# Kernel tuning notes

Hardware: AMD Instinct MI355X
Metric: run time of the kernel (lower is better)

Reference implementation:

```python
import jax, jax.numpy as jnp
import numpy as np

PATCH = 4
WINDOW = 4
MAX_ROUNDS = 4
MIN_ROUNDS = 2
LAMBDA_P = 0.2
TOPK = 8


def _ln(x, g, b, eps=1e-5):
    m = x.mean(-1, keepdims=True)
    v = ((x - m) ** 2).mean(-1, keepdims=True)
    return (x - m) / jnp.sqrt(v + eps) * g + b


def _mlp(x, w1, b1, w2, b2):
    # Linear -> exact GELU -> Linear (matches nn.GELU default)
    return jax.nn.gelu(x @ w1 + b1, approximate=False) @ w2 + b2


def setup_inputs() -> dict:
    key = jax.random.key(0)
    ks = jax.random.split(key, 24)
    B, T, D, V = 16, 4096, 256, 256
    s = 0.02
    w = lambda i, shape: jax.random.normal(ks[i], shape, jnp.float32) * s
    z = lambda *shape: jnp.zeros(shape, jnp.float32)
    o = lambda *shape: jnp.ones(shape, jnp.float32)
    return {
        'x': jax.random.randint(ks[0], (B, T), 0, V),
        'emb': w(1, (V, D)), 'pos': w(2, (PATCH, D)),
        'gru_wih': w(3, (D, 3 * D)), 'gru_whh': w(4, (D, 3 * D)),
        'gru_bih': z(3 * D), 'gru_bhh': z(3 * D),
        'ln_p_g': o(D), 'ln_p_b': z(D),
        'sum_w': w(5, (D, D)), 'sum_b': z(D),
        'msg_w1': w(6, (2 * D, D)), 'msg_b1': z(D), 'msg_w2': w(7, (D, D)), 'msg_b2': z(D),
        'upd_w1': w(8, (2 * D, D)), 'upd_b1': z(D), 'upd_w2': w(9, (D, D)), 'upd_b2': z(D),
        'halt_w': w(10, (D, 1)), 'halt_b': z(1),
        'ln_mp_g': o(D), 'ln_mp_b': z(D),
        'q_w': w(11, (D, D)), 'q_b': z(D),
        'k_w': w(12, (D, D)), 'k_b': z(D),
        'v_w': w(13, (D, D)), 'v_b': z(D),
        'o_w': w(14, (D, D)), 'o_b': z(D),
        'bc_w': w(15, (D, D)), 'bc_b': z(D),
        'ln_f_g': o(D), 'ln_f_b': z(D),
        'head_w': w(16, (D, V)),
    }


def reference(x, emb, pos, gru_wih, gru_whh, gru_bih, gru_bhh, ln_p_g, ln_p_b,
              sum_w, sum_b, msg_w1, msg_b1, msg_w2, msg_b2, upd_w1, upd_b1,
              upd_w2, upd_b2, halt_w, halt_b, ln_mp_g, ln_mp_b, q_w, q_b,
              k_w, k_b, v_w, v_b, o_w, o_b, bc_w, bc_b, ln_f_g, ln_f_b, head_w):
    B, T = x.shape
    D = emb.shape[1]
    Np = T // PATCH  # T is divisible by PATCH for these shapes (no pad needed)

    # --- GRU patch processor over B*Np sequences of length PATCH ---
    tok = x.reshape(B * Np, PATCH)
    hseq = emb[tok] + pos[None]  # [BN, P, D]

    def gru_step(h, xt):
        gi = xt @ gru_wih + gru_bih
        gh = h @ gru_whh + gru_bhh
        ir, iz, inn = jnp.split(gi, 3, -1)
        hr, hz, hn = jnp.split(gh, 3, -1)
        r = jax.nn.sigmoid(ir + hr)
        zz = jax.nn.sigmoid(iz + hz)
        n = jnp.tanh(inn + r * hn)
        h = (1 - zz) * n + zz * h
        return h, h

    h0 = jnp.zeros((B * Np, D), hseq.dtype)
    _, gout = jax.lax.scan(gru_step, h0, jnp.swapaxes(hseq, 0, 1))
    local = _ln(jnp.swapaxes(gout, 0, 1), ln_p_g, ln_p_b).reshape(B, Np, PATCH, D)
    summaries = local.mean(2) @ sum_w + sum_b  # [B, Np, D]

    # --- Local message passing with ACT-style halting (fixed MAX_ROUNDS) ---
    h = summaries
    remaining = jnp.ones((B, Np, 1), h.dtype)
    out_mp = jnp.zeros_like(h)
    kl = jnp.zeros((), h.dtype)
    for step in range(MAX_ROUNDS):
        padded = jnp.pad(h, ((0, 0), (WINDOW, 0), (0, 0)))
        # neighbors: self plus previous WINDOW patches -> [B, Np, W+1, D]
        neigh = jnp.stack([padded[:, WINDOW - w:WINDOW - w + Np] for w in range(WINDOW + 1)], axis=2)
        self_exp = jnp.broadcast_to(h[:, :, None, :], neigh.shape)
        msgs = _mlp(jnp.concatenate([self_exp, neigh], -1), msg_w1, msg_b1, msg_w2, msg_b2).mean(2)
        h = _ln(h + _mlp(jnp.concatenate([h, msgs], -1), upd_w1, upd_b1, upd_w2, upd_b2), ln_mp_g, ln_mp_b)
        if step < MIN_ROUNDS:
            hp = jnp.zeros((B, Np, 1), h.dtype)
        else:
            hp = jax.nn.sigmoid(h.mean(1, keepdims=True) @ halt_w + halt_b)  # [B,1,1]
            hp = jnp.broadcast_to(hp, (B, Np, 1))
        if step == MAX_ROUNDS - 1:
            hp = jnp.ones_like(hp)
        out_mp = out_mp + remaining * hp * h
        remaining = remaining * (1 - hp)
        p_geom = LAMBDA_P * (1 - LAMBDA_P) ** step
        # F.kl_div(log(mean+eps), log(p_geom), log_target=True) = p*(log p - log(mean+eps))
        kl = kl + p_geom * (np.log(p_geom) - jnp.log(hp.mean() + 1e-8))
    kl = kl / MAX_ROUNDS

    # --- Sparse top-k causal retrieval ---
    q = out_mp @ q_w + q_b
    kk = out_mp @ k_w + k_b
    v = out_mp @ v_w + v_b
    scores = jnp.einsum('bnd,bmd->bnm', q, kk) / np.sqrt(D).astype(np.float32)
    causal = jnp.tril(jnp.ones((Np, Np), bool))
    neg = jnp.asarray(-jnp.inf, scores.dtype)
    scores = jnp.where(causal[None], scores, neg)
    vals, idx = jax.lax.top_k(scores, TOPK)  # [B, Np, k]
    bi = jnp.arange(B)[:, None, None]
    ni = jnp.arange(Np)[None, :, None]
    sparse = jnp.full_like(scores, neg).at[bi, ni, idx].set(vals)
    attn = jax.nn.softmax(sparse, axis=-1)
    retrieved = jnp.einsum('bnm,bmd->bnd', attn, v) @ o_w + o_b

    # --- Broadcast back to tokens and project ---
    combined = out_mp + retrieved
    broad = combined @ bc_w + bc_b
    final = (local + broad[:, :, None, :]).reshape(B, Np * PATCH, D)[:, :T]
    logits = _ln(final, ln_f_g, ln_f_b) @ head_w
    return logits, kl
```

## Files before the change

### kernel.cpp

```cpp
#include <hip/hip_runtime.h>
#include <math.h>


typedef __bf16 bf16_t;
typedef bf16_t bf16x8 __attribute__((ext_vector_type(8)));
typedef bf16_t bf16x4 __attribute__((ext_vector_type(4)));
typedef float f32x4 __attribute__((ext_vector_type(4)));

#define GF_BIAS 1
#define GF_GELU 4
#define GF_RES 8
#define GF_F32OUT 32

__device__ __forceinline__ float gelu_exact(float x) {
  return 0.5f * x * (1.0f + erff(x * 0.7071067811865475f));
}

__device__ __forceinline__ float sigm(float x) { return 1.f / (1.f + expf(-x)); }

__device__ __forceinline__ float wave_sum(float v) {
#pragma unroll
  for (int o = 32; o; o >>= 1) v += __shfl_xor(v, o, 64);
  return v;
}

__device__ __forceinline__ void gload16(const void* g, void* l) {
  __builtin_amdgcn_global_load_lds(
      (const __attribute__((address_space(1))) void*)g,
      (__attribute__((address_space(3))) void*)l, 16, 0, 0);
}

__device__ __forceinline__ unsigned long long skey(float s, int m) {
  unsigned u = __float_as_uint(s);
  u ^= (u & 0x80000000u) ? 0xFFFFFFFFu : 0x80000000u;
  return ((unsigned long long)u << 32) | (unsigned)(0x7FFFFFFF - m);
}

template<int FLAGS>
__global__ __launch_bounds__(256)
void gemm_bt(const bf16_t* __restrict__ A, const bf16_t* __restrict__ Bt,
             void* __restrict__ Cv, const float* __restrict__ bias,
             const bf16_t* __restrict__ res,
             int lda, int ldb, int ldc, int ldr)
{
  __shared__ __align__(16) bf16_t As[128][64];
  __shared__ __align__(16) bf16_t Bs[128][64];
  const int m0 = blockIdx.x * 128, n0 = blockIdx.y * 128;
  const int tid = threadIdx.x, lane = tid & 63, wave = tid >> 6;
  const int wm = (wave >> 1) << 6, wn = (wave & 1) << 6;
  const int lr = lane & 15, lg = lane >> 4;
  const int cx = lane & 7;

  const int srow = wave * 32 + (lane >> 3);
  const int scol = (((lane & 7) ^ ((lane >> 3) & 7)) * 8);
  const bf16_t* ga = A  + (long long)(m0 + srow) * lda + scol;
  const bf16_t* gb = Bt + (long long)(n0 + srow) * ldb + scol;
  char* lA = (char*)(&As[srow][0]) + (lane & 7) * 16;
  char* lB = (char*)(&Bs[srow][0]) + (lane & 7) * 16;

  f32x4 acc[4][4] = {};

#pragma unroll
  for (int kt = 0; kt < 4; kt++) {
    const int ko = kt * 64;
#pragma unroll
    for (int q = 0; q < 4; q++) {
      gload16(ga + (long long)q * 8 * lda + ko, lA + q * 1024);
      gload16(gb + (long long)q * 8 * ldb + ko, lB + q * 1024);
    }
    __syncthreads();
#pragma unroll
    for (int kk = 0; kk < 2; kk++) {
      const int co = ((kk * 4 + lg) ^ cx) << 4;
      bf16x8 af[4], bfv[4];
#pragma unroll
      for (int i = 0; i < 4; i++)
        af[i]  = *(const bf16x8*)((char*)As + (wm + i * 16 + lr) * 128 + co);
#pragma unroll
      for (int j = 0; j < 4; j++)
        bfv[j] = *(const bf16x8*)((char*)Bs + (wn + j * 16 + lr) * 128 + co);
#pragma unroll
      for (int i = 0; i < 4; i++)
#pragma unroll
        for (int j = 0; j < 4; j++)
          acc[i][j] = __builtin_amdgcn_mfma_f32_16x16x32_bf16(af[i], bfv[j], acc[i][j], 0, 0, 0);
    }
    if (kt < 3) __syncthreads();
  }

#pragma unroll
  for (int i = 0; i < 4; i++) {
#pragma unroll
    for (int j = 0; j < 4; j++) {
      const int col = n0 + wn + j * 16 + lr;
      const float bval = (FLAGS & GF_BIAS) ? bias[col] : 0.f;
#pragma unroll
      for (int e = 0; e < 4; e++) {
        const int row = m0 + wm + i * 16 + lg * 4 + e;
        float v = acc[i][j][e] + bval;
        if (FLAGS & GF_RES) v += (float)res[(long long)row * ldr + col];
        if (FLAGS & GF_GELU) v = gelu_exact(v);
        const long long ci = (long long)row * ldc + col;
        if (FLAGS & GF_F32OUT) ((float*)Cv)[ci] = v;
        else                   ((bf16_t*)Cv)[ci] = (bf16_t)v;
      }
    }
  }
}

template<int FLAGS>
__global__ __launch_bounds__(256)
void gemm64(const bf16_t* __restrict__ A, const bf16_t* __restrict__ Bt,
            void* __restrict__ Cv, const float* __restrict__ bias,
            const bf16_t* __restrict__ res,
            int lda, int ldb, int ldc, int ldr)
{
  __shared__ __align__(16) bf16_t As[64][64];
  __shared__ __align__(16) bf16_t Bs[64][64];
  const int m0 = blockIdx.x * 64, n0 = blockIdx.y * 64;
  const int tid = threadIdx.x, lane = tid & 63, wave = tid >> 6;
  const int wm = (wave >> 1) * 32, wn = (wave & 1) * 32;
  const int lr = lane & 15, lg = lane >> 4;
  const int cx = lane & 7;

  const int srow = tid >> 3;
  const int scol = (((tid & 7) ^ (srow & 7)) * 8);
  const bf16_t* ga = A  + (long long)(m0 + srow) * lda + scol;
  const bf16_t* gb = Bt + (long long)(n0 + srow) * ldb + scol;
  char* lA = (char*)As + tid * 16;
  char* lB = (char*)Bs + tid * 16;

  f32x4 acc[2][2] = {};

#pragma unroll
  for (int kt = 0; kt < 4; kt++) {
    const int ko = kt * 64;
    gload16(ga + ko, lA);
    gload16(ga + 32LL * lda + ko, lA + 4096);
    gload16(gb + ko, lB);
    gload16(gb + 32LL * ldb + ko, lB + 4096);
    __syncthreads();
#pragma unroll
    for (int kk = 0; kk < 2; kk++) {
      const int co = ((kk * 4 + lg) ^ cx) << 4;
      bf16x8 af[2], bfv[2];
#pragma unroll
      for (int i = 0; i < 2; i++)
        af[i]  = *(const bf16x8*)((char*)As + (wm + i * 16 + lr) * 128 + co);
#pragma unroll
      for (int j = 0; j < 2; j++)
        bfv[j] = *(const bf16x8*)((char*)Bs + (wn + j * 16 + lr) * 128 + co);
#pragma unroll
      for (int i = 0; i < 2; i++)
#pragma unroll
        for (int j = 0; j < 2; j++)
          acc[i][j] = __builtin_amdgcn_mfma_f32_16x16x32_bf16(af[i], bfv[j], acc[i][j], 0, 0, 0);
    }
    if (kt < 3) __syncthreads();
  }

#pragma unroll
  for (int i = 0; i < 2; i++) {
#pragma unroll
    for (int j = 0; j < 2; j++) {
      const int col = n0 + wn + j * 16 + lr;
      const float bval = (FLAGS & GF_BIAS) ? bias[col] : 0.f;
#pragma unroll
      for (int e = 0; e < 4; e++) {
        const int row = m0 + wm + i * 16 + lg * 4 + e;
        float v = acc[i][j][e] + bval;
        if (FLAGS & GF_RES) v += (float)res[(long long)row * ldr + col];
        if (FLAGS & GF_GELU) v = gelu_exact(v);
        const long long ci = (long long)row * ldc + col;
        if (FLAGS & GF_F32OUT) ((float*)Cv)[ci] = v;
        else                   ((bf16_t*)Cv)[ci] = (bf16_t)v;
      }
    }
  }
}

__global__ __launch_bounds__(64)
void k_fatopk(const bf16_t* __restrict__ QKV, bf16_t* __restrict__ O) {
  const int b = blockIdx.y;
  const int qw = (int)((blockIdx.x + ((blockIdx.y * 21) & 63)) & 63);
  const int lane = threadIdx.x;
  const int lr = lane & 15, lg = lane >> 4;
  const bf16_t* Qp = QKV + (long long)b * (1024LL * 768);
  const bf16_t* Kp = Qp + 256;
  const bf16_t* Vp = Qp + 512;
  const int q0 = qw * 16;
  const int qrow = q0 + lr;

  bf16x8 bq[8];
#pragma unroll
  for (int s = 0; s < 8; s++)
    bq[s] = *(const bf16x8*)(Qp + (long long)qrow * 768 + s * 32 + lg * 8);

  unsigned long long kv[8] = {0ull, 0ull, 0ull, 0ull, 0ull, 0ull, 0ull, 0ull};

#define INS8(KEY) {                                                     \
    const unsigned long long k_ = (KEY);                                \
    if (k_ > kv[7]) {                                                   \
      kv[7] = k_;                                                       \
      _Pragma("unroll")                                                 \
      for (int j_ = 7; j_ > 0; j_--)                                    \
        if (kv[j_] > kv[j_-1]) {                                        \
          const unsigned long long t_ = kv[j_];                         \
          kv[j_] = kv[j_-1]; kv[j_-1] = t_;                             \
        }                                                               \
    }                                                                   \
  }

  const int klim = qw + 1;
  for (int kt = 0; kt < klim; kt += 2) {
    const int kt2 = (kt + 1 < klim) ? kt + 1 : kt;
    const bf16_t* ka = Kp + (long long)(kt  * 16 + lr) * 768 + lg * 8;
    const bf16_t* kb = Kp + (long long)(kt2 * 16 + lr) * 768 + lg * 8;
    bf16x8 afA[8], afB[8];
#pragma unroll
    for (int s = 0; s < 8; s++) afA[s] = *(const bf16x8*)(ka + s * 32);
#pragma unroll
    for (int s = 0; s < 8; s++) afB[s] = *(const bf16x8*)(kb + s * 32);
    f32x4 a0 = {}, a1 = {};
#pragma unroll
    for (int s = 0; s < 8; s += 2) {
      a0 = __builtin_amdgcn_mfma_f32_16x16x32_bf16(afA[s],     bq[s],     a0, 0, 0, 0);
      a1 = __builtin_amdgcn_mfma_f32_16x16x32_bf16(afA[s + 1], bq[s + 1], a1, 0, 0, 0);
    }
#pragma unroll
    for (int e = 0; e < 4; e++) {
      const int m = kt * 16 + lg * 4 + e;
      if (m <= qrow) INS8(skey((a0[e] + a1[e]) * 0.0625f, m));
    }
    if (kt2 != kt) {
      f32x4 b0 = {}, b1 = {};
#pragma unroll
      for (int s = 0; s < 8; s += 2) {
        b0 = __builtin_amdgcn_mfma_f32_16x16x32_bf16(afB[s],     bq[s],     b0, 0, 0, 0);
        b1 = __builtin_amdgcn_mfma_f32_16x16x32_bf16(afB[s + 1], bq[s + 1], b1, 0, 0, 0);
      }
#pragma unroll
      for (int e = 0; e < 4; e++) {
        const int m = kt2 * 16 + lg * 4 + e;
        if (m <= qrow) INS8(skey((b0[e] + b1[e]) * 0.0625f, m));
      }
    }
  }
#undef INS8

  float wv[8]; int wi[8];
#pragma unroll
  for (int r = 0; r < 8; r++) {
    unsigned long long mk = kv[0];
    unsigned long long ok = __shfl_xor(mk, 16, 64); if (ok > mk) mk = ok;
    ok = __shfl_xor(mk, 32, 64); if (ok > mk) mk = ok;
    if (mk != 0ull) {
      unsigned hi = (unsigned)(mk >> 32);
      hi ^= (hi & 0x80000000u) ? 0x80000000u : 0xFFFFFFFFu;
      wv[r] = __uint_as_float(hi);
      wi[r] = 0x7FFFFFFF - (int)(unsigned)(mk & 0xFFFFFFFFu);
    } else {
      wv[r] = 0.f; wi[r] = -1;
    }
    if (kv[0] == mk && mk != 0ull) {
#pragma unroll
      for (int j = 0; j < 7; j++) kv[j] = kv[j + 1];
      kv[7] = 0ull;
    }
  }

  const float mx = wv[0];
  float w8[8]; float den = 0.f;
#pragma unroll
  for (int j = 0; j < 8; j++) {
    w8[j] = (wi[j] >= 0) ? expf(wv[j] - mx) : 0.f;
    den += w8[j];
  }
  const float inv = 1.f / den;

  f32x4 av[16] = {};
#pragma unroll
  for (int j = 0; j < 8; j++) {
    if (wi[j] >= 0) {
      const float wj = w8[j] * inv;
      const bf16_t* vr = Vp + (long long)wi[j] * 768 + lg * 64;
#pragma unroll
      for (int c = 0; c < 8; c++) {
        const bf16x8 vv = *(const bf16x8*)(vr + c * 8);
#pragma unroll
        for (int e = 0; e < 4; e++) {
          av[2 * c][e]     = fmaf(wj, (float)vv[e],     av[2 * c][e]);
          av[2 * c + 1][e] = fmaf(wj, (float)vv[4 + e], av[2 * c + 1][e]);
        }
      }
    }
  }
  bf16_t* op = O + ((long long)b * 1024 + qrow) * 256 + lg * 64;
#pragma unroll
  for (int c = 0; c < 8; c++) {
    bf16x8 ov;
#pragma unroll
    for (int e = 0; e < 4; e++) {
      ov[e]     = (bf16_t)av[2 * c][e];
      ov[4 + e] = (bf16_t)av[2 * c + 1][e];
    }
    *(bf16x8*)(op + c * 8) = ov;
  }
}

struct TD { const float* src; bf16_t* dst; int N; int k0; int ld; };
struct PrepArgs {
  TD d[16];
  const float* emb; const float* pos; bf16_t* XE;
  const float* msg_b1; const float* msg_b2; const float* upd_w1; const float* upd_b1;
  const float* q_b; const float* k_b; const float* v_b;
  float* BIAS3; float* QKVB;
};

__global__ __launch_bounds__(256) void k_prep(PrepArgs pa) {
  const int y = blockIdx.y, x = blockIdx.x, d = threadIdx.x;
  if (y < 16) {
    TD t = pa.d[y];
    if (x >= t.N) return;
    if (t.k0 < 0) t.dst[(long long)x * 256 + d] = (bf16_t)t.src[(long long)x * t.ld + d];
    else          t.dst[(long long)x * 256 + d] = (bf16_t)t.src[(long long)(t.k0 + d) * t.ld + x];
  } else if (y == 16) {
    const int p = x >> 8, v = x & 255;
    pa.XE[(long long)x * 256 + d] = (bf16_t)(pa.emb[v * 256 + d] + pa.pos[p * 256 + d]);
  } else {
    if      (x == 0) pa.BIAS3[d] = pa.msg_b1[d];
    else if (x == 1) pa.BIAS3[256 + d] = 0.f;
    else if (x == 2) {
      float acc = pa.upd_b1[d];
      for (int k = 0; k < 256; k++) acc += pa.msg_b2[k] * pa.upd_w1[(long long)(256 + k) * 256 + d];
      pa.BIAS3[512 + d] = acc;
    }
    else if (x == 3) pa.QKVB[d] = pa.q_b[d];
    else if (x == 4) pa.QKVB[256 + d] = pa.k_b[d];
    else if (x == 5) pa.QKVB[512 + d] = pa.v_b[d];
  }
}

__global__ __launch_bounds__(64)
void k_gru_gate(const int* __restrict__ x, const bf16_t* __restrict__ gitab,
                const bf16_t* __restrict__ GH, const float* __restrict__ bhh,
                bf16_t* __restrict__ H, bf16_t* __restrict__ LOC, int t)
{
  const int s = blockIdx.x, lane = threadIdx.x, d0 = lane * 4;
  const int v = x[s * 4 + t];
  const bf16_t* gi = gitab + (long long)(t * 256 + v) * 768;
  const bf16x4 g_r = *(const bf16x4*)(gi + d0);
  const bf16x4 g_z = *(const bf16x4*)(gi + 256 + d0);
  const bf16x4 g_n = *(const bf16x4*)(gi + 512 + d0);
  float hr[4], hz[4], hn[4], hp[4];
  if (t == 0) {
#pragma unroll
    for (int e = 0; e < 4; e++) {
      hr[e] = bhh[d0 + e]; hz[e] = bhh[256 + d0 + e]; hn[e] = bhh[512 + d0 + e];
      hp[e] = 0.f;
    }
  } else {
    const bf16_t* gh = GH + (long long)s * 768;
    const bf16x4 a = *(const bf16x4*)(gh + d0);
    const bf16x4 b4 = *(const bf16x4*)(gh + 256 + d0);
    const bf16x4 c4 = *(const bf16x4*)(gh + 512 + d0);
    const bf16x4 hv = *(const bf16x4*)(H + (long long)s * 256 + d0);
#pragma unroll
    for (int e = 0; e < 4; e++) { hr[e] = a[e]; hz[e] = b4[e]; hn[e] = c4[e]; hp[e] = hv[e]; }
  }
  bf16x4 ho;
#pragma unroll
  for (int e = 0; e < 4; e++) {
    const float r = sigm((float)g_r[e] + hr[e]);
    const float zz = sigm((float)g_z[e] + hz[e]);
    const float nn = tanhf((float)g_n[e] + r * hn[e]);
    ho[e] = (bf16_t)((1.f - zz) * nn + zz * hp[e]);
  }
  *(bf16x4*)(H + (long long)s * 256 + d0) = ho;
  *(bf16x4*)(LOC + ((long long)s * 4 + t) * 256 + d0) = ho;
}

__global__ __launch_bounds__(64)
void k_ln(const bf16_t* __restrict__ X, const bf16_t* __restrict__ ADD, int addmode,
          bf16_t* __restrict__ OUT, const float* __restrict__ g,
          const float* __restrict__ b)
{
  const long long r = blockIdx.x;
  const int d0 = threadIdx.x * 4;
  const bf16x4 xv = *(const bf16x4*)(X + r * 256 + d0);
  float xf[4];
#pragma unroll
  for (int e = 0; e < 4; e++) xf[e] = (float)xv[e];
  if (addmode == 1) {
    const bf16x4 av = *(const bf16x4*)(ADD + r * 256 + d0);
#pragma unroll
    for (int e = 0; e < 4; e++) xf[e] += (float)av[e];
  } else if (addmode == 2) {
    const bf16x4 av = *(const bf16x4*)(ADD + (r >> 2) * 256 + d0);
#pragma unroll
    for (int e = 0; e < 4; e++) xf[e] += (float)av[e];
  }
  const float mean = wave_sum(xf[0] + xf[1] + xf[2] + xf[3]) * (1.f / 256.f);
  float q = 0.f;
#pragma unroll
  for (int e = 0; e < 4; e++) { const float dx = xf[e] - mean; q += dx * dx; }
  const float rstd = rsqrtf(wave_sum(q) * (1.f / 256.f) + 1e-5f);
  const float4 gv = *(const float4*)(g + d0);
  const float4 bv = *(const float4*)(b + d0);
  const float gg[4] = {gv.x, gv.y, gv.z, gv.w};
  const float bb[4] = {bv.x, bv.y, bv.z, bv.w};
  bf16x4 ov;
#pragma unroll
  for (int e = 0; e < 4; e++) ov[e] = (bf16_t)((xf[e] - mean) * rstd * gg[e] + bb[e]);
  *(bf16x4*)(OUT + r * 256 + d0) = ov;
}

__global__ __launch_bounds__(64)
void k_lnp4(bf16_t* __restrict__ LOC, bf16_t* __restrict__ SUMB,
            const float* __restrict__ g, const float* __restrict__ b)
{
  const long long s = blockIdx.x;
  const int d0 = threadIdx.x * 4;
  const float4 gv = *(const float4*)(g + d0);
  const float4 bv = *(const float4*)(b + d0);
  const float gg[4] = {gv.x, gv.y, gv.z, gv.w};
  const float bb[4] = {bv.x, bv.y, bv.z, bv.w};
  float accd[4] = {0.f, 0.f, 0.f, 0.f};
#pragma unroll
  for (int t = 0; t < 4; t++) {
    bf16_t* row = LOC + (s * 4 + t) * 256 + d0;
    const bf16x4 xv = *(const bf16x4*)row;
    float xf[4];
#pragma unroll
    for (int e = 0; e < 4; e++) xf[e] = (float)xv[e];
    const float mean = wave_sum(xf[0] + xf[1] + xf[2] + xf[3]) * (1.f / 256.f);
    float q = 0.f;
#pragma unroll
    for (int e = 0; e < 4; e++) { const float dx = xf[e] - mean; q += dx * dx; }
    const float rstd = rsqrtf(wave_sum(q) * (1.f / 256.f) + 1e-5f);
    bf16x4 ov;
#pragma unroll
    for (int e = 0; e < 4; e++) {
      const float y = (xf[e] - mean) * rstd * gg[e] + bb[e];
      ov[e] = (bf16_t)y;
      accd[e] += y;
    }
    *(bf16x4*)row = ov;
  }
  bf16x4 sv;
#pragma unroll
  for (int e = 0; e < 4; e++) sv[e] = (bf16_t)(accd[e] * 0.25f);
  *(bf16x4*)(SUMB + s * 256 + d0) = sv;
}

__global__ __launch_bounds__(64)
void k_gelumix(const bf16_t* __restrict__ A3, bf16_t* __restrict__ G)
{
  const long long s = blockIdx.x;
  const int n = (int)(s & 1023);
  const int d0 = threadIdx.x * 4;
  const bf16x4 av = *(const bf16x4*)(A3 + s * 768 + d0);
  float a[4];
#pragma unroll
  for (int e = 0; e < 4; e++) a[e] = (float)av[e];
  float acc[4] = {0.f, 0.f, 0.f, 0.f};
  const bf16_t* bbase = A3 + s * 768 + 256 + d0;
#pragma unroll
  for (int w = 0; w <= 4; w++) {
    if (n >= w) {
      const bf16x4 bn = *(const bf16x4*)(bbase - (long long)w * 768);
#pragma unroll
      for (int e = 0; e < 4; e++) acc[e] += gelu_exact(a[e] + (float)bn[e]);
    } else {
#pragma unroll
      for (int e = 0; e < 4; e++) acc[e] += gelu_exact(a[e]);
    }
  }
  bf16x4 ov;
#pragma unroll
  for (int e = 0; e < 4; e++) ov[e] = (bf16_t)(acc[e] * 0.2f);
  *(bf16x4*)(G + s * 256 + d0) = ov;
}

__global__ __launch_bounds__(64)
void k_halt1(const bf16_t* __restrict__ Hm, float* __restrict__ PS) {
  const int c = blockIdx.x, b = blockIdx.y, d0 = threadIdx.x * 4;
  float acc[4] = {0.f, 0.f, 0.f, 0.f};
  const bf16_t* base = Hm + ((long long)b * 1024 + c * 32) * 256 + d0;
#pragma unroll 4
  for (int n = 0; n < 32; n++) {
    const bf16x4 hv = *(const bf16x4*)(base + (long long)n * 256);
#pragma unroll
    for (int e = 0; e < 4; e++) acc[e] += (float)hv[e];
  }
  float4 o4; o4.x = acc[0]; o4.y = acc[1]; o4.z = acc[2]; o4.w = acc[3];
  *(float4*)(PS + ((long long)b * 32 + c) * 256 + d0) = o4;
}

__global__ __launch_bounds__(64)
void k_halt2(const float* __restrict__ PS, const float* __restrict__ hw,
             const float* __restrict__ hb, float* __restrict__ HP) {
  const int b = blockIdx.x, d0 = threadIdx.x * 4;
  float acc[4] = {0.f, 0.f, 0.f, 0.f};
  for (int c = 0; c < 32; c++) {
    const float4 p4 = *(const float4*)(PS + ((long long)b * 32 + c) * 256 + d0);
    acc[0] += p4.x; acc[1] += p4.y; acc[2] += p4.z; acc[3] += p4.w;
  }
  const float4 w4 = *(const float4*)(hw + d0);
  float val = (acc[0] * w4.x + acc[1] * w4.y + acc[2] * w4.z + acc[3] * w4.w) * (1.f / 1024.f);
  val = wave_sum(val);
  if (threadIdx.x == 0) HP[b] = sigm(val + hb[0]);
}

__global__ void k_kl(const float* __restrict__ HP, float* __restrict__ out) {
  float s = 0.f;
  for (int b = 0; b < 16; b++) s += HP[b];
  const float hpm = s * (1.f / 16.f);
  const float l8 = logf(1e-8f);
  const float p0 = 0.2f, p1 = 0.16f, p2 = 0.128f, p3 = 0.1024f;
  const float kl = p0 * (logf(p0) - l8)
                 + p1 * (logf(p1) - l8)
                 + p2 * (logf(p2) - logf(hpm + 1e-8f))
                 + p3 * (logf(p3) - logf(1.f + 1e-8f));
  out[0] = kl * 0.25f;
}

__global__ __launch_bounds__(64)
void k_outmp(const bf16_t* __restrict__ Hm, const float* __restrict__ HP,
             bf16_t* __restrict__ O, int acc) {
  const long long s = blockIdx.x;
  const int d0 = threadIdx.x * 4;
  const int b = (int)(s >> 10);
  const float hp = HP[b];
  const bf16x4 hv = *(const bf16x4*)(Hm + s * 256 + d0);
  bf16x4 ov;
  if (acc) {
    const bf16x4 pv = *(const bf16x4*)(O + s * 256 + d0);
#pragma unroll
    for (int e = 0; e < 4; e++) ov[e] = (bf16_t)((float)pv[e] + (1.f - hp) * (float)hv[e]);
  } else {
#pragma unroll
    for (int e = 0; e < 4; e++) ov[e] = (bf16_t)(hp * (float)hv[e]);
  }
  *(bf16x4*)(O + s * 256 + d0) = ov;
}

extern "C" void kernel_launch(void* const* d_in, const int* in_sizes, int n_in,
                              void* d_out, int out_size, void* d_ws, size_t ws_size,
                              hipStream_t stream) {
  (void)in_sizes; (void)n_in; (void)ws_size;
  const int*   x      = (const int*)d_in[0];
  const float* emb    = (const float*)d_in[1];
  const float* pos    = (const float*)d_in[2];
  const float* wih    = (const float*)d_in[3];
  const float* whh    = (const float*)d_in[4];
  const float* bih    = (const float*)d_in[5];
  const float* bhh    = (const float*)d_in[6];
  const float* lnp_g  = (const float*)d_in[7];
  const float* lnp_b  = (const float*)d_in[8];
  const float* sum_w  = (const float*)d_in[9];
  const float* sum_b  = (const float*)d_in[10];
  const float* msg_w1 = (const float*)d_in[11];
  const float* msg_b1 = (const float*)d_in[12];
  const float* msg_w2 = (const float*)d_in[13];
  const float* msg_b2 = (const float*)d_in[14];
  const float* upd_w1 = (const float*)d_in[15];
  const float* upd_b1 = (const float*)d_in[16];
  const float* upd_w2 = (const float*)d_in[17];
  const float* upd_b2 = (const float*)d_in[18];
  const float* halt_w = (const float*)d_in[19];
  const float* halt_b = (const float*)d_in[20];
  const float* lnm_g  = (const float*)d_in[21];
  const float* lnm_b  = (const float*)d_in[22];
  const float* q_b    = (const float*)d_in[24];
  const float* k_b    = (const float*)d_in[26];
  const float* v_b    = (const float*)d_in[28];
  const float* o_b    = (const float*)d_in[30];
  const float* bc_b   = (const float*)d_in[32];
  const float* lnf_g  = (const float*)d_in[33];
  const float* lnf_b  = (const float*)d_in[34];

  char* base = (char*)d_ws;
  size_t off = 0;
  auto alloc = [&](size_t bytes) -> void* {
    void* p = (void*)(base + off);
    off += (bytes + 255) & ~(size_t)255;
    return p;
  };
  const size_t SL2 = 16384ull * 256 * 2;
  bf16_t* WIHT  = (bf16_t*)alloc(768 * 256 * 2);
  bf16_t* WHHT  = (bf16_t*)alloc(768 * 256 * 2);
  bf16_t* SUMT  = (bf16_t*)alloc(256 * 256 * 2);
  bf16_t* MW    = (bf16_t*)alloc(768 * 256 * 2);
  bf16_t* W2T   = (bf16_t*)alloc(256 * 256 * 2);
  bf16_t* W2NT  = (bf16_t*)alloc(256 * 256 * 2);
  bf16_t* UW1MT = (bf16_t*)alloc(256 * 256 * 2);
  bf16_t* UW2T  = (bf16_t*)alloc(256 * 256 * 2);
  bf16_t* WCB   = (bf16_t*)alloc(256 * 256 * 2);
  bf16_t* QKVW  = (bf16_t*)alloc(768 * 256 * 2);
  bf16_t* OT    = (bf16_t*)alloc(256 * 256 * 2);
  bf16_t* BCT   = (bf16_t*)alloc(256 * 256 * 2);
  bf16_t* HEADT = (bf16_t*)alloc(256 * 256 * 2);
  float*  BIAS3 = (float*)alloc(768 * 4);
  float*  QKVB  = (float*)alloc(768 * 4);
  bf16_t* XE    = (bf16_t*)alloc(1024ull * 256 * 2);
  bf16_t* GITAB = (bf16_t*)alloc(1024ull * 768 * 2);
  bf16_t* LOCb  = (bf16_t*)alloc(65536ull * 256 * 2);

  char*   SCR   = (char*)alloc(16ull * 1024 * 1024 * 4);
  bf16_t* GH    = (bf16_t*)SCR;
  bf16_t* H     = (bf16_t*)(SCR + 25165824);
  bf16_t* SUMB  = (bf16_t*)(SCR + 33554432);
  bf16_t* A3    = (bf16_t*)(SCR + 41943040);

  bf16_t* HMP   = (bf16_t*)alloc(SL2);
  bf16_t* G     = (bf16_t*)alloc(SL2);
  bf16_t* BROAD = (bf16_t*)alloc(SL2);
  bf16_t* UB    = (bf16_t*)alloc(SL2);
  bf16_t* U2B   = (bf16_t*)alloc(SL2);
  bf16_t* OUTMP = (bf16_t*)alloc(SL2);
  bf16_t* QKV   = (bf16_t*)alloc(16384ull * 768 * 2);
  float*  PS    = (float*)alloc(512ull * 256 * 4);
  float*  HP    = (float*)alloc(64);
  bf16_t* ATT   = UB;
  bf16_t* COMB  = U2B;
  float*  out   = (float*)d_out;
  float*  klout = out + (out_size - 1);

  PrepArgs pa;
  pa.d[0]  = { wih,                    WIHT,            768, 0,   768 };
  pa.d[1]  = { whh,                    WHHT,            768, 0,   768 };
  pa.d[2]  = { sum_w,                  SUMT,            256, 0,   256 };
  pa.d[3]  = { msg_w1,                 MW,              256, 0,   256 };
  pa.d[4]  = { msg_w1,                 MW + 256 * 256,  256, 256, 256 };
  pa.d[5]  = { upd_w1,                 MW + 512 * 256,  256, 0,   256 };
  pa.d[6]  = { msg_w2,                 W2T,             256, 0,   256 };
  pa.d[7]  = { upd_w1,                 UW1MT,           256, 256, 256 };
  pa.d[8]  = { upd_w2,                 UW2T,            256, 0,   256 };
  pa.d[9]  = { (const float*)d_in[23], QKVW,            256, 0,   256 };
  pa.d[10] = { (const float*)d_in[25], QKVW + 256*256,  256, 0,   256 };
  pa.d[11] = { (const float*)d_in[27], QKVW + 512*256,  256, 0,   256 };
  pa.d[12] = { (const float*)d_in[29], OT,              256, 0,   256 };
  pa.d[13] = { (const float*)d_in[31], BCT,             256, 0,   256 };
  pa.d[14] = { (const float*)d_in[35], HEADT,           256, 0,   256 };
  pa.d[15] = { msg_w2,                 W2NT,            256, -1,  256 };
  pa.emb = emb; pa.pos = pos; pa.XE = XE;
  pa.msg_b1 = msg_b1; pa.msg_b2 = msg_b2; pa.upd_w1 = upd_w1; pa.upd_b1 = upd_b1;
  pa.q_b = q_b; pa.k_b = k_b; pa.v_b = v_b;
  pa.BIAS3 = BIAS3; pa.QKVB = QKVB;
  k_prep<<<dim3(1024, 18), 256, 0, stream>>>(pa);

  gemm64<0><<<dim3(4, 4), 256, 0, stream>>>(
      UW1MT, W2NT, WCB, nullptr, nullptr, 256, 256, 256, 0);

  gemm64<GF_BIAS><<<dim3(16, 12), 256, 0, stream>>>(
      XE, WIHT, GITAB, bih, nullptr, 256, 256, 768, 0);

  k_gru_gate<<<16384, 64, 0, stream>>>(x, GITAB, GH, bhh, H, LOCb, 0);
  for (int t = 1; t < 4; t++) {
    gemm_bt<GF_BIAS><<<dim3(128, 6), 256, 0, stream>>>(
        H, WHHT, GH, bhh, nullptr, 256, 256, 768, 0);
    k_gru_gate<<<16384, 64, 0, stream>>>(x, GITAB, GH, bhh, H, LOCb, t);
  }

  k_lnp4<<<16384, 64, 0, stream>>>(LOCb, SUMB, lnp_g, lnp_b);
  gemm64<GF_BIAS><<<dim3(256, 4), 256, 0, stream>>>(
      SUMB, SUMT, HMP, sum_b, nullptr, 256, 256, 256, 0);

  for (int step = 0; step < 4; step++) {
    gemm_bt<GF_BIAS><<<dim3(128, 6), 256, 0, stream>>>(
        HMP, MW, A3, BIAS3, nullptr, 256, 256, 768, 0);
    k_gelumix<<<16384, 64, 0, stream>>>(A3, G);
    gemm64<GF_RES | GF_GELU><<<dim3(256, 4), 256, 0, stream>>>(
        G, WCB, UB, nullptr, A3 + 512, 256, 256, 256, 768);
    gemm64<GF_BIAS><<<dim3(256, 4), 256, 0, stream>>>(
        UB, UW2T, U2B, upd_b2, nullptr, 256, 256, 256, 0);
    k_ln<<<16384, 64, 0, stream>>>(HMP, U2B, 1, HMP, lnm_g, lnm_b);
    if (step == 2) {
      k_halt1<<<dim3(32, 16), 64, 0, stream>>>(HMP, PS);
      k_halt2<<<16, 64, 0, stream>>>(PS, halt_w, halt_b, HP);
      k_kl<<<1, 1, 0, stream>>>(HP, klout);
      k_outmp<<<16384, 64, 0, stream>>>(HMP, HP, OUTMP, 0);
    } else if (step == 3) {
      k_outmp<<<16384, 64, 0, stream>>>(HMP, HP, OUTMP, 1);
    }
  }

  gemm_bt<GF_BIAS><<<dim3(128, 6), 256, 0, stream>>>(
      OUTMP, QKVW, QKV, QKVB, nullptr, 256, 256, 768, 0);
  k_fatopk<<<dim3(64, 16), 64, 0, stream>>>(QKV, ATT);
  gemm64<GF_BIAS | GF_RES><<<dim3(256, 4), 256, 0, stream>>>(
      ATT, OT, COMB, o_b, OUTMP, 256, 256, 256, 256);
  gemm64<GF_BIAS><<<dim3(256, 4), 256, 0, stream>>>(
      COMB, BCT, BROAD, bc_b, nullptr, 256, 256, 256, 0);

  k_ln<<<65536, 64, 0, stream>>>(LOCb, BROAD, 2, LOCb, lnf_g, lnf_b);
  gemm_bt<GF_F32OUT><<<dim3(512, 2), 256, 0, stream>>>(
      LOCb, HEADT, out, nullptr, nullptr, 256, 256, 256, 0);
}
```

Measured before the change: 487.5 us.

## Split top-k attention key scan across four waves and fuse final layer-norm with output mix

The top-k retrieval kernel now runs four waves per 16-query block. Each wave scans an interleaved subset of key tiles and keeps its own top-8 candidates, and the per-wave lists are merged through shared memory by one wave. The value gather is then spread across all 256 threads. This shortens the serial causal key loop, which is badly load-imbalanced for late query blocks. Separately, the last message-passing step fuses its layer norm with the out_mp accumulation, so the HMP write and reread plus one launch are dropped. The cost is extra syncthreads and shared-memory merge work.

```diff
diff --git a/kernel.cpp b/kernel.cpp
--- a/kernel.cpp
+++ b/kernel.cpp
@@ -179,11 +179,16 @@
   }
 }
 
-__global__ __launch_bounds__(64)
+__global__ __launch_bounds__(256)
 void k_fatopk(const bf16_t* __restrict__ QKV, bf16_t* __restrict__ O) {
+  __shared__ unsigned long long cand[4][16][8];
+  __shared__ float wrow[16][8];
+  __shared__ int   irow[16][8];
   const int b = blockIdx.y;
-  const int qw = (int)((blockIdx.x + ((blockIdx.y * 21) & 63)) & 63);
-  const int lane = threadIdx.x;
+  const int qw = (int)((blockIdx.x + ((unsigned)(b * 21) & 63u)) & 63u);
+  const int tid = threadIdx.x;
+  const int wid = tid >> 6;
+  const int lane = tid & 63;
   const int lr = lane & 15, lg = lane >> 4;
   const bf16_t* Qp = QKV + (long long)b * (1024LL * 768);
   const bf16_t* Kp = Qp + 256;
@@ -212,100 +217,110 @@
   }
 
   const int klim = qw + 1;
-  for (int kt = 0; kt < klim; kt += 2) {
-    const int kt2 = (kt + 1 < klim) ? kt + 1 : kt;
-    const bf16_t* ka = Kp + (long long)(kt  * 16 + lr) * 768 + lg * 8;
-    const bf16_t* kb = Kp + (long long)(kt2 * 16 + lr) * 768 + lg * 8;
-    bf16x8 afA[8], afB[8];
-#pragma unroll
-    for (int s = 0; s < 8; s++) afA[s] = *(const bf16x8*)(ka + s * 32);
-#pragma unroll
-    for (int s = 0; s < 8; s++) afB[s] = *(const bf16x8*)(kb + s * 32);
+  for (int kt = wid; kt < klim; kt += 4) {
+    const bf16_t* ka = Kp + (long long)(kt * 16 + lr) * 768 + lg * 8;
+    bf16x8 af[8];
+#pragma unroll
+    for (int s = 0; s < 8; s++) af[s] = *(const bf16x8*)(ka + s * 32);
     f32x4 a0 = {}, a1 = {};
 #pragma unroll
     for (int s = 0; s < 8; s += 2) {
-      a0 = __builtin_amdgcn_mfma_f32_16x16x32_bf16(afA[s],     bq[s],     a0, 0, 0, 0);
-      a1 = __builtin_amdgcn_mfma_f32_16x16x32_bf16(afA[s + 1], bq[s + 1], a1, 0, 0, 0);
+      a0 = __builtin_amdgcn_mfma_f32_16x16x32_bf16(af[s],     bq[s],     a0, 0, 0, 0);
+      a1 = __builtin_amdgcn_mfma_f32_16x16x32_bf16(af[s + 1], bq[s + 1], a1, 0, 0, 0);
     }
 #pragma unroll
     for (int e = 0; e < 4; e++) {
       const int m = kt * 16 + lg * 4 + e;
       if (m <= qrow) INS8(skey((a0[e] + a1[e]) * 0.0625f, m));
     }
-    if (kt2 != kt) {
-      f32x4 b0 = {}, b1 = {};
-#pragma unroll
-      for (int s = 0; s < 8; s += 2) {
-        b0 = __builtin_amdgcn_mfma_f32_16x16x32_bf16(afB[s],     bq[s],     b0, 0, 0, 0);
-        b1 = __builtin_amdgcn_mfma_f32_16x16x32_bf16(afB[s + 1], bq[s + 1], b1, 0, 0, 0);
-      }
-#pragma unroll
-      for (int e = 0; e < 4; e++) {
-        const int m = kt2 * 16 + lg * 4 + e;
-        if (m <= qrow) INS8(skey((b0[e] + b1[e]) * 0.0625f, m));
-      }
-    }
   }
 #undef INS8
 
-  float wv[8]; int wi[8];
 #pragma unroll
   for (int r = 0; r < 8; r++) {
     unsigned long long mk = kv[0];
     unsigned long long ok = __shfl_xor(mk, 16, 64); if (ok > mk) mk = ok;
     ok = __shfl_xor(mk, 32, 64); if (ok > mk) mk = ok;
-    if (mk != 0ull) {
-      unsigned hi = (unsigned)(mk >> 32);
-      hi ^= (hi & 0x80000000u) ? 0x80000000u : 0xFFFFFFFFu;
-      wv[r] = __uint_as_float(hi);
-      wi[r] = 0x7FFFFFFF - (int)(unsigned)(mk & 0xFFFFFFFFu);
-    } else {
-      wv[r] = 0.f; wi[r] = -1;
-    }
+    if (lg == 0) cand[wid][lr][r] = mk;
     if (kv[0] == mk && mk != 0ull) {
 #pragma unroll
       for (int j = 0; j < 7; j++) kv[j] = kv[j + 1];
       kv[7] = 0ull;
     }
   }
-
-  const float mx = wv[0];
-  float w8[8]; float den = 0.f;
+  __syncthreads();
+
+  if (wid == 0) {
+    unsigned long long kv2[8];
+#pragma unroll
+    for (int j = 0; j < 8; j++) kv2[j] = cand[lg][lr][j];
+    float wv[8]; int wi[8];
+#pragma unroll
+    for (int r = 0; r < 8; r++) {
+      unsigned long long mk = kv2[0];
+      unsigned long long ok = __shfl_xor(mk, 16, 64); if (ok > mk) mk = ok;
+      ok = __shfl_xor(mk, 32, 64); if (ok > mk) mk = ok;
+      if (mk != 0ull) {
+        unsigned hi = (unsigned)(mk >> 32);
+        hi ^= (hi & 0x80000000u) ? 0x80000000u : 0xFFFFFFFFu;
+        wv[r] = __uint_as_float(hi);
+        wi[r] = 0x7FFFFFFF - (int)(unsigned)(mk & 0xFFFFFFFFu);
+      } else {
+        wv[r] = 0.f; wi[r] = -1;
+      }
+      if (kv2[0] == mk && mk != 0ull) {
+#pragma unroll
+        for (int j = 0; j < 7; j++) kv2[j] = kv2[j + 1];
+        kv2[7] = 0ull;
+      }
+    }
+    const float mx = wv[0];
+    float w8[8]; float den = 0.f;
+#pragma unroll
+    for (int j = 0; j < 8; j++) {
+      w8[j] = (wi[j] >= 0) ? expf(wv[j] - mx) : 0.f;
+      den += w8[j];
+    }
+    const float inv = 1.f / den;
+    if (lg == 0) {
+#pragma unroll
+      for (int j = 0; j < 8; j++) {
+        wrow[lr][j] = w8[j] * inv;
+        irow[lr][j] = wi[j];
+      }
+    }
+  }
+  __syncthreads();
+
+  const int rr = wid * 4 + lg;
+  const int c0 = (lane & 15) * 16;
+  f32x4 av[4] = {};
 #pragma unroll
   for (int j = 0; j < 8; j++) {
-    w8[j] = (wi[j] >= 0) ? expf(wv[j] - mx) : 0.f;
-    den += w8[j];
-  }
-  const float inv = 1.f / den;
-
-  f32x4 av[16] = {};
-#pragma unroll
-  for (int j = 0; j < 8; j++) {
-    if (wi[j] >= 0) {
-      const float wj = w8[j] * inv;
-      const bf16_t* vr = Vp + (long long)wi[j] * 768 + lg * 64;
-#pragma unroll
-      for (int c = 0; c < 8; c++) {
-        const bf16x8 vv = *(const bf16x8*)(vr + c * 8);
-#pragma unroll
-        for (int e = 0; e < 4; e++) {
-          av[2 * c][e]     = fmaf(wj, (float)vv[e],     av[2 * c][e]);
-          av[2 * c + 1][e] = fmaf(wj, (float)vv[4 + e], av[2 * c + 1][e]);
-        }
+    const int idx = irow[rr][j];
+    if (idx >= 0) {
+      const float wj = wrow[rr][j];
+      const bf16_t* vr = Vp + (long long)idx * 768 + c0;
+      const bf16x8 v0 = *(const bf16x8*)vr;
+      const bf16x8 v1 = *(const bf16x8*)(vr + 8);
+#pragma unroll
+      for (int e = 0; e < 4; e++) {
+        av[0][e] = fmaf(wj, (float)v0[e],     av[0][e]);
+        av[1][e] = fmaf(wj, (float)v0[4 + e], av[1][e]);
+        av[2][e] = fmaf(wj, (float)v1[e],     av[2][e]);
+        av[3][e] = fmaf(wj, (float)v1[4 + e], av[3][e]);
       }
     }
   }
-  bf16_t* op = O + ((long long)b * 1024 + qrow) * 256 + lg * 64;
-#pragma unroll
-  for (int c = 0; c < 8; c++) {
-    bf16x8 ov;
-#pragma unroll
-    for (int e = 0; e < 4; e++) {
-      ov[e]     = (bf16_t)av[2 * c][e];
-      ov[4 + e] = (bf16_t)av[2 * c + 1][e];
-    }
-    *(bf16x8*)(op + c * 8) = ov;
-  }
+  bf16_t* op = O + ((long long)b * 1024 + q0 + rr) * 256 + c0;
+  bf16x8 o0, o1;
+#pragma unroll
+  for (int e = 0; e < 4; e++) {
+    o0[e] = (bf16_t)av[0][e]; o0[4 + e] = (bf16_t)av[1][e];
+    o1[e] = (bf16_t)av[2][e]; o1[4 + e] = (bf16_t)av[3][e];
+  }
+  *(bf16x8*)op = o0;
+  *(bf16x8*)(op + 8) = o1;
 }
 
 struct TD { const float* src; bf16_t* dst; int N; int k0; int ld; };
@@ -413,6 +428,38 @@
 #pragma unroll
   for (int e = 0; e < 4; e++) ov[e] = (bf16_t)((xf[e] - mean) * rstd * gg[e] + bb[e]);
   *(bf16x4*)(OUT + r * 256 + d0) = ov;
+}
+
+__global__ __launch_bounds__(64)
+void k_ln_out(const bf16_t* __restrict__ X, const bf16_t* __restrict__ ADD,
+              bf16_t* __restrict__ OUTMP, const float* __restrict__ HP,
+              const float* __restrict__ g, const float* __restrict__ b)
+{
+  const long long r = blockIdx.x;
+  const int d0 = threadIdx.x * 4;
+  const bf16x4 xv = *(const bf16x4*)(X + r * 256 + d0);
+  const bf16x4 avv = *(const bf16x4*)(ADD + r * 256 + d0);
+  float xf[4];
+#pragma unroll
+  for (int e = 0; e < 4; e++) xf[e] = (float)xv[e] + (float)avv[e];
+  const float mean = wave_sum(xf[0] + xf[1] + xf[2] + xf[3]) * (1.f / 256.f);
+  float q = 0.f;
+#pragma unroll
+  for (int e = 0; e < 4; e++) { const float dx = xf[e] - mean; q += dx * dx; }
+  const float rstd = rsqrtf(wave_sum(q) * (1.f / 256.f) + 1e-5f);
+  const float4 gv = *(const float4*)(g + d0);
+  const float4 bv = *(const float4*)(b + d0);
+  const float gg[4] = {gv.x, gv.y, gv.z, gv.w};
+  const float bb[4] = {bv.x, bv.y, bv.z, bv.w};
+  const float rem = 1.f - HP[(int)(r >> 10)];
+  const bf16x4 pv = *(const bf16x4*)(OUTMP + r * 256 + d0);
+  bf16x4 ov;
+#pragma unroll
+  for (int e = 0; e < 4; e++) {
+    const float y = (xf[e] - mean) * rstd * gg[e] + bb[e];
+    ov[e] = (bf16_t)((float)pv[e] + rem * y);
+  }
+  *(bf16x4*)(OUTMP + r * 256 + d0) = ov;
 }
 
 __global__ __launch_bounds__(64)
@@ -675,20 +722,22 @@
         G, WCB, UB, nullptr, A3 + 512, 256, 256, 256, 768);
     gemm64<GF_BIAS><<<dim3(256, 4), 256, 0, stream>>>(
         UB, UW2T, U2B, upd_b2, nullptr, 256, 256, 256, 0);
-    k_ln<<<16384, 64, 0, stream>>>(HMP, U2B, 1, HMP, lnm_g, lnm_b);
-    if (step == 2) {
-      k_halt1<<<dim3(32, 16), 64, 0, stream>>>(HMP, PS);
-      k_halt2<<<16, 64, 0, stream>>>(PS, halt_w, halt_b, HP);
-      k_kl<<<1, 1, 0, stream>>>(HP, klout);
-      k_outmp<<<16384, 64, 0, stream>>>(HMP, HP, OUTMP, 0);
-    } else if (step == 3) {
-      k_outmp<<<16384, 64, 0, stream>>>(HMP, HP, OUTMP, 1);
+    if (step == 3) {
+      k_ln_out<<<16384, 64, 0, stream>>>(HMP, U2B, OUTMP, HP, lnm_g, lnm_b);
+    } else {
+      k_ln<<<16384, 64, 0, stream>>>(HMP, U2B, 1, HMP, lnm_g, lnm_b);
+      if (step == 2) {
+        k_halt1<<<dim3(32, 16), 64, 0, stream>>>(HMP, PS);
+        k_halt2<<<16, 64, 0, stream>>>(PS, halt_w, halt_b, HP);
+        k_kl<<<1, 1, 0, stream>>>(HP, klout);
+        k_outmp<<<16384, 64, 0, stream>>>(HMP, HP, OUTMP, 0);
+      }
     }
   }
 
   gemm_bt<GF_BIAS><<<dim3(128, 6), 256, 0, stream>>>(
       OUTMP, QKVW, QKV, QKVB, nullptr, 256, 256, 768, 0);
-  k_fatopk<<<dim3(64, 16), 64, 0, stream>>>(QKV, ATT);
+  k_fatopk<<<dim3(64, 16), 256, 0, stream>>>(QKV, ATT);
   gemm64<GF_BIAS | GF_RES><<<dim3(256, 4), 256, 0, stream>>>(
       ATT, OT, COMB, o_b, OUTMP, 256, 256, 256, 256);
   gemm64<GF_BIAS><<<dim3(256, 4), 256, 0, stream>>>(
```

New measurement: 467.9 us. 1.04x faster.
